# Performance work log

Measured on AMD Instinct MI355X. Metric: run time of the kernel, lower is better.

## Reference

```python
import jax, jax.numpy as jnp
import numpy as np

TOP_K = 2
NUM_MOE_LAYERS = 12


def _gemma_mlp(x, gate_w, up_w, down_w):
    # GemmaMLP: down( gelu_tanh(gate(x)) * up(x) )
    g = jnp.einsum('bsh,hi->bsi', x, gate_w)
    u = jnp.einsum('bsh,hi->bsi', x, up_w)
    return jnp.einsum('bsi,ih->bsh', jax.nn.gelu(g, approximate=True) * u, down_w)


def setup_inputs() -> dict:
    key = jax.random.key(0)
    ks = jax.random.split(key, 8)
    B, S, H, I, E = 32, 256, 1024, 4096, 8  # batch, seq, hidden, intermediate, skill experts
    std = 0.02
    return {
        'x': jax.random.normal(ks[0], (B, S, H), jnp.float32),
        'router_logits': jax.random.normal(ks[1], (B, E), jnp.float32),
        'skill_gate': jax.random.normal(ks[2], (E, H, I), jnp.float32) * std,
        'skill_up': jax.random.normal(ks[3], (E, H, I), jnp.float32) * std,
        'skill_down': jax.random.normal(ks[4], (E, I, H), jnp.float32) * std,
        'shared_gate': jax.random.normal(ks[5], (H, I), jnp.float32) * std,
        'shared_up': jax.random.normal(ks[6], (H, I), jnp.float32) * std,
        'shared_down': jax.random.normal(ks[7], (I, H), jnp.float32) * std,
    }


def reference(x, router_logits, skill_gate, skill_up, skill_down,
              shared_gate, shared_up, shared_down):
    B = x.shape[0]
    E = skill_gate.shape[0]
    # top-k softmax routing (per sequence), renormalized over selected experts
    rw = jax.nn.softmax(router_logits.astype(jnp.float32), axis=-1)
    w, sel = jax.lax.top_k(rw, TOP_K)                      # [B, k]
    w = w / w.sum(axis=-1, keepdims=True)
    w = w.astype(x.dtype)
    # ScaleGradient: identity fwd, grad scaled by 1/num_moe_layers
    scale = 1.0 / NUM_MOE_LAYERS
    w = scale * w + (1.0 - scale) * jax.lax.stop_gradient(w)
    # dense combine weights [B, E]; zero weight == not routed (same math as gather/scatter)
    dense_w = jnp.zeros((B, E), x.dtype).at[jnp.arange(B)[:, None], sel].add(w)

    def step(acc, params):
        g, u, d, we = params                               # we: [B]
        return acc + we[:, None, None] * _gemma_mlp(x, g, u, d), None

    out, _ = jax.lax.scan(step, jnp.zeros_like(x),
                          (skill_gate, skill_up, skill_down, dense_w.T))
    out = out + _gemma_mlp(x, shared_gate, shared_up, shared_down)
    return out
```

## Files before the change

kernel.cpp:

```cpp
#include <hip/hip_runtime.h>

typedef __bf16 bf16x8 __attribute__((ext_vector_type(8)));
typedef float  f32x4  __attribute__((ext_vector_type(4)));

__device__ __forceinline__ unsigned short f2bf(float f) {
    unsigned u = __float_as_uint(f);
    u += 0x7fffu + ((u >> 16) & 1u);
    return (unsigned short)(u >> 16);
}

__device__ __forceinline__ void gld_lds16(const void* g, void* l) {
    __builtin_amdgcn_global_load_lds(
        (const __attribute__((address_space(1))) void*)g,
        (__attribute__((address_space(3))) void*)l,
        16, 0, 0);
}

#define WAITVM(N) asm volatile("s_waitcnt vmcnt(" #N ")" ::: "memory")

#define NB  32
#define SQ  256
#define HD  1024
#define ID  4096
#define NEXP 8
#define PAIRS (NB * 3)

#define OFF_EID    ((size_t)0)
#define OFF_WGT    ((size_t)512)
#define OFF_XBF    ((size_t)1024)
#define OFF_GATET  (OFF_XBF   + (size_t)16777216)
#define OFF_UPT    (OFF_GATET + (size_t)75497472)
#define OFF_DOWNT  (OFF_UPT   + (size_t)75497472)
#define OFF_ACT    (OFF_DOWNT + (size_t)75497472)

__global__ void routing_kernel(const float* __restrict__ logits,
                               int* __restrict__ eid, float* __restrict__ wgt) {
    int b = threadIdx.x;
    if (b < NB) {
        float l[NEXP];
        for (int j = 0; j < NEXP; ++j) l[j] = logits[b * NEXP + j];
        int a0 = 0;
        for (int j = 1; j < NEXP; ++j) if (l[j] > l[a0]) a0 = j;
        int a1 = -1;
        for (int j = 0; j < NEXP; ++j) {
            if (j == a0) continue;
            if (a1 < 0 || l[j] > l[a1]) a1 = j;
        }
        float w0 = 1.0f / (1.0f + expf(l[a1] - l[a0]));
        eid[b * 3 + 0] = a0;  wgt[b * 3 + 0] = w0;
        eid[b * 3 + 1] = a1;  wgt[b * 3 + 1] = 1.0f - w0;
        eid[b * 3 + 2] = NEXP; wgt[b * 3 + 2] = 1.0f;
    }
}

__global__ void xcvt_kernel(const float* __restrict__ x,
                            unsigned short* __restrict__ xb, int n4) {
    int i = blockIdx.x * 256 + threadIdx.x;
    if (i < n4) {
        float4 v = ((const float4*)x)[i];
        union { unsigned short s[4]; uint2 u; } p;
        p.s[0] = f2bf(v.x); p.s[1] = f2bf(v.y);
        p.s[2] = f2bf(v.z); p.s[3] = f2bf(v.w);
        ((uint2*)xb)[i] = p.u;
    }
}

__global__ void transpose_cvt(const float* __restrict__ skill,
                              const float* __restrict__ shared_m,
                              unsigned short* __restrict__ out, int R, int C) {
    const int e = blockIdx.z;
    const float* src = (e < NEXP) ? (skill + (size_t)e * R * C) : shared_m;
    unsigned short* dst = out + (size_t)e * R * C;
    const int c0 = blockIdx.x * 64;
    const int r0 = blockIdx.y * 64;
    __shared__ unsigned short t[64][66];
    const int tid = threadIdx.x;
    const int lr = tid >> 4;
    const int lc = (tid & 15) * 4;
    for (int it = 0; it < 4; ++it) {
        int r = lr + it * 16;
        float4 v = *(const float4*)(src + (size_t)(r0 + r) * C + c0 + lc);
        t[r][lc + 0] = f2bf(v.x);
        t[r][lc + 1] = f2bf(v.y);
        t[r][lc + 2] = f2bf(v.z);
        t[r][lc + 3] = f2bf(v.w);
    }
    __syncthreads();
    const int oc = tid >> 2;
    const int k0 = (tid & 3) * 16;
    unsigned int pk[8];
    for (int j = 0; j < 8; ++j) {
        unsigned int lo = t[k0 + 2 * j + 0][oc];
        unsigned int hi = t[k0 + 2 * j + 1][oc];
        pk[j] = lo | (hi << 16);
    }
    unsigned short* dp = dst + (size_t)(c0 + oc) * R + r0 + k0;
    ((uint4*)dp)[0] = make_uint4(pk[0], pk[1], pk[2], pk[3]);
    ((uint4*)dp)[1] = make_uint4(pk[4], pk[5], pk[6], pk[7]);
}

__global__ __launch_bounds__(512, 2) void stage1_gateup(
    const unsigned short* __restrict__ xbf,
    const unsigned short* __restrict__ gateT,
    const unsigned short* __restrict__ upT,
    const int* __restrict__ eid, const float* __restrict__ wgt,
    unsigned short* __restrict__ act)
{
    extern __shared__ unsigned short lds[];

    const int lid = blockIdx.x;
    const int swz = (lid & 7) * 768 + (lid >> 3);
    const int nt  = swz & 31;
    const int mt  = (swz >> 5) & 1;
    const int p   = swz >> 6;
    const int b   = p / 3;
    const int e   = eid[p];
    const float wS = wgt[p];

    const int tid  = threadIdx.x;
    const int wv   = tid >> 6;
    const int lane = tid & 63;
    const int wr   = wv >> 2;
    const int wc   = wv & 3;

    const int lhi  = lane >> 3;
    const int llo  = lane & 7;
    const int csw8 = (llo ^ lhi) * 8;
    const int w2   = wv * 2;

    const size_t lofs = (size_t)(wv * 16 + lhi) * HD + csw8;
    const unsigned short* pA = xbf   + (size_t)(b * SQ + mt * 128) * HD + lofs;
    const unsigned short* pG = gateT + ((size_t)e * ID + nt * 128) * HD + lofs;
    const unsigned short* pU = upT   + ((size_t)e * ID + nt * 128) * HD + lofs;

    const int lrow = lane & 15;
    const int kq   = (lane >> 4) * 8;
    const int xt   = (lrow & 7) << 3;
    const int c0s  = kq ^ xt;
    const int c1s  = (32 + kq) ^ xt;
    const int rA0  = (wr * 64 + lrow) * 64;
    const int rG0  = (wc * 32 + lrow) * 64;

    f32x4 accg[4][2], accu[4][2];
#pragma unroll
    for (int i = 0; i < 4; ++i)
#pragma unroll
        for (int j = 0; j < 2; ++j) { accg[i][j] = (f32x4)0.f; accu[i][j] = (f32x4)0.f; }

    const int NT = HD / 64;

#pragma unroll
    for (int t0 = 0; t0 < 2; ++t0) {
        unsigned short* Lb = lds + t0 * 24576;
#pragma unroll
        for (int q = 0; q < 2; ++q) {
            const size_t o = (size_t)t0 * 64 + (size_t)q * (8 * HD);
            gld_lds16(pA + o, Lb +         (w2 + q) * 512);
            gld_lds16(pG + o, Lb +  8192 + (w2 + q) * 512);
            gld_lds16(pU + o, Lb + 16384 + (w2 + q) * 512);
        }
    }

    int cur = 0, tgt = 2;
#pragma unroll 1
    for (int t = 0; t < NT; ++t) {
        __builtin_amdgcn_sched_barrier(0);
        unsigned short* Lc = lds + cur * 24576;
        unsigned short* Lt = lds + tgt * 24576;
        const bool pf = (t + 2 < NT);
        const size_t kp = (size_t)(t + 2) * 64;
        if (pf) {
            gld_lds16(pA + kp, Lt +         w2 * 512);
            gld_lds16(pG + kp, Lt +  8192 + w2 * 512);
            gld_lds16(pU + kp, Lt + 16384 + w2 * 512);
            WAITVM(9);
        } else if (t + 1 < NT) {
            WAITVM(6);
        } else {
            WAITVM(0);
        }
        __builtin_amdgcn_s_barrier();
        __builtin_amdgcn_sched_barrier(0);

        {
            bf16x8 af[4], gf[2], uf[2];
#pragma unroll
            for (int mf = 0; mf < 4; ++mf)
                af[mf] = *(const bf16x8*)(Lc + rA0 + mf * 1024 + c0s);
#pragma unroll
            for (int nf = 0; nf < 2; ++nf) {
                gf[nf] = *(const bf16x8*)(Lc +  8192 + rG0 + nf * 1024 + c0s);
                uf[nf] = *(const bf16x8*)(Lc + 16384 + rG0 + nf * 1024 + c0s);
            }
            __builtin_amdgcn_s_setprio(1);
#pragma unroll
            for (int mf = 0; mf < 4; ++mf)
#pragma unroll
                for (int nf = 0; nf < 2; ++nf) {
                    accg[mf][nf] = __builtin_amdgcn_mfma_f32_16x16x32_bf16(af[mf], gf[nf], accg[mf][nf], 0, 0, 0);
                    accu[mf][nf] = __builtin_amdgcn_mfma_f32_16x16x32_bf16(af[mf], uf[nf], accu[mf][nf], 0, 0, 0);
                }
            __builtin_amdgcn_s_setprio(0);
        }
        __builtin_amdgcn_s_barrier();

        {
            bf16x8 af[4], gf[2], uf[2];
#pragma unroll
            for (int mf = 0; mf < 4; ++mf)
                af[mf] = *(const bf16x8*)(Lc + rA0 + mf * 1024 + c1s);
#pragma unroll
            for (int nf = 0; nf < 2; ++nf) {
                gf[nf] = *(const bf16x8*)(Lc +  8192 + rG0 + nf * 1024 + c1s);
                uf[nf] = *(const bf16x8*)(Lc + 16384 + rG0 + nf * 1024 + c1s);
            }
            if (pf) {
                gld_lds16(pA + kp + 8 * HD, Lt +         (w2 + 1) * 512);
                gld_lds16(pG + kp + 8 * HD, Lt +  8192 + (w2 + 1) * 512);
                gld_lds16(pU + kp + 8 * HD, Lt + 16384 + (w2 + 1) * 512);
            }
            __builtin_amdgcn_s_setprio(1);
#pragma unroll
            for (int mf = 0; mf < 4; ++mf)
#pragma unroll
                for (int nf = 0; nf < 2; ++nf) {
                    accg[mf][nf] = __builtin_amdgcn_mfma_f32_16x16x32_bf16(af[mf], gf[nf], accg[mf][nf], 0, 0, 0);
                    accu[mf][nf] = __builtin_amdgcn_mfma_f32_16x16x32_bf16(af[mf], uf[nf], accu[mf][nf], 0, 0, 0);
                }
            __builtin_amdgcn_s_setprio(0);
        }
        __builtin_amdgcn_s_barrier();

        cur = (cur == 2) ? 0 : cur + 1;
        tgt = (tgt == 2) ? 0 : tgt + 1;
    }

    unsigned short* actp = act + (size_t)p * (SQ * ID);
    const int rb = mt * 128 + wr * 64 + ((lane >> 4) << 2);
    const int cb = nt * 128 + wc * 32 + (lane & 15);
#pragma unroll
    for (int mf = 0; mf < 4; ++mf)
#pragma unroll
        for (int nf = 0; nf < 2; ++nf)
#pragma unroll
            for (int r = 0; r < 4; ++r) {
                float g = accg[mf][nf][r];
                float u = accu[mf][nf][r];
                float tt = 0.7978845608028654f * (g + 0.044715f * g * g * g);
                float h = 0.5f * g * (1.0f + tanhf(tt)) * u * wS;
                actp[(size_t)(rb + mf * 16 + r) * ID + cb + nf * 16] = f2bf(h);
            }
}

__global__ __launch_bounds__(512, 2) void stage2_down(
    const unsigned short* __restrict__ act,
    const unsigned short* __restrict__ downT,
    const int* __restrict__ eid,
    float* __restrict__ out)
{
    extern __shared__ unsigned short lds[];

    const int lid = blockIdx.x;
    const int swz = (lid & 7) * 32 + (lid >> 3);
    const int nt  = swz & 3;
    const int mt  = (swz >> 2) & 1;
    const int b   = swz >> 3;
    const int b3  = b * 3;
    const int e0 = eid[b3], e1 = eid[b3 + 1], e2 = eid[b3 + 2];

    const int tid  = threadIdx.x;
    const int wv   = tid >> 6;
    const int lane = tid & 63;
    const int wr   = wv >> 2;
    const int wc   = wv & 3;

    const int lhi  = lane >> 3;
    const int llo  = lane & 7;
    const int csw8 = (llo ^ lhi) * 8;
    const int w2   = wv * 2, w4 = wv * 4;

    const size_t laneA = (size_t)(wv * 16 + lhi) * ID + csw8;
    const size_t laneB = (size_t)(wv * 32 + lhi) * ID + csw8;

    const int lrow = lane & 15;
    const int kq   = (lane >> 4) * 8;
    const int xt   = (lrow & 7) << 3;
    const int c0s  = kq ^ xt;
    const int c1s  = (32 + kq) ^ xt;
    const int rA0  = (wr * 64 + lrow) * 64;
    const int rB0  = (wc * 64 + lrow) * 64;

    f32x4 acc[4][4];
#pragma unroll
    for (int i = 0; i < 4; ++i)
#pragma unroll
        for (int j = 0; j < 4; ++j) acc[i][j] = (f32x4)0.f;

    const int NT = 3 * ID / 64;

    auto srcAB = [&](int tt, const unsigned short*& A, const unsigned short*& B) {
        const int slot = tt >> 6;
        const int i0   = (tt & 63) << 6;
        const int esl  = (slot == 0) ? e0 : ((slot == 1) ? e1 : e2);
        A = act   + ((size_t)(b3 + slot) * SQ + mt * 128) * ID + i0 + laneA;
        B = downT + ((size_t)esl * HD + nt * 256) * ID + i0 + laneB;
    };

#pragma unroll
    for (int t0 = 0; t0 < 2; ++t0) {
        const unsigned short *A, *B;
        srcAB(t0, A, B);
        unsigned short* Lb = lds + t0 * 24576;
#pragma unroll
        for (int q = 0; q < 2; ++q)
            gld_lds16(A + (size_t)q * (8 * ID), Lb + (w2 + q) * 512);
#pragma unroll
        for (int q = 0; q < 4; ++q)
            gld_lds16(B + (size_t)q * (8 * ID), Lb + 8192 + (w4 + q) * 512);
    }

    int cur = 0, tgt = 2;
#pragma unroll 1
    for (int t = 0; t < NT; ++t) {
        __builtin_amdgcn_sched_barrier(0);
        unsigned short* Lc = lds + cur * 24576;
        unsigned short* Lt = lds + tgt * 24576;
        const bool pf = (t + 2 < NT);
        const unsigned short *SA = nullptr, *SB = nullptr;
        if (pf) {
            srcAB(t + 2, SA, SB);
            gld_lds16(SA,                    Lt +        w2 * 512);
            gld_lds16(SA + (size_t)(8 * ID), Lt +        (w2 + 1) * 512);
            gld_lds16(SB,                    Lt + 8192 + w4 * 512);
            WAITVM(9);
        } else if (t + 1 < NT) {
            WAITVM(6);
        } else {
            WAITVM(0);
        }
        __builtin_amdgcn_s_barrier();
        __builtin_amdgcn_sched_barrier(0);

        {
            bf16x8 af[4], bfr[4];
#pragma unroll
            for (int mf = 0; mf < 4; ++mf)
                af[mf] = *(const bf16x8*)(Lc + rA0 + mf * 1024 + c0s);
#pragma unroll
            for (int nf = 0; nf < 4; ++nf)
                bfr[nf] = *(const bf16x8*)(Lc + 8192 + rB0 + nf * 1024 + c0s);
            __builtin_amdgcn_s_setprio(1);
#pragma unroll
            for (int mf = 0; mf < 4; ++mf)
#pragma unroll
                for (int nf = 0; nf < 4; ++nf)
                    acc[mf][nf] = __builtin_amdgcn_mfma_f32_16x16x32_bf16(af[mf], bfr[nf], acc[mf][nf], 0, 0, 0);
            __builtin_amdgcn_s_setprio(0);
        }
        __builtin_amdgcn_s_barrier();

        {
            bf16x8 af[4], bfr[4];
#pragma unroll
            for (int mf = 0; mf < 4; ++mf)
                af[mf] = *(const bf16x8*)(Lc + rA0 + mf * 1024 + c1s);
#pragma unroll
            for (int nf = 0; nf < 4; ++nf)
                bfr[nf] = *(const bf16x8*)(Lc + 8192 + rB0 + nf * 1024 + c1s);
            if (pf) {
                gld_lds16(SB + (size_t)(8  * ID), Lt + 8192 + (w4 + 1) * 512);
                gld_lds16(SB + (size_t)(16 * ID), Lt + 8192 + (w4 + 2) * 512);
                gld_lds16(SB + (size_t)(24 * ID), Lt + 8192 + (w4 + 3) * 512);
            }
            __builtin_amdgcn_s_setprio(1);
#pragma unroll
            for (int mf = 0; mf < 4; ++mf)
#pragma unroll
                for (int nf = 0; nf < 4; ++nf)
                    acc[mf][nf] = __builtin_amdgcn_mfma_f32_16x16x32_bf16(af[mf], bfr[nf], acc[mf][nf], 0, 0, 0);
            __builtin_amdgcn_s_setprio(0);
        }
        __builtin_amdgcn_s_barrier();

        cur = (cur == 2) ? 0 : cur + 1;
        tgt = (tgt == 2) ? 0 : tgt + 1;
    }

    const int rb  = mt * 128 + wr * 64 + ((lane >> 4) << 2);
    const int cbN = nt * 256 + wc * 64 + (lane & 15);
#pragma unroll
    for (int mf = 0; mf < 4; ++mf)
#pragma unroll
        for (int nf = 0; nf < 4; ++nf)
#pragma unroll
            for (int r = 0; r < 4; ++r)
                out[((size_t)b * SQ + rb + mf * 16 + r) * HD + cbN + nf * 16] = acc[mf][nf][r];
}

extern "C" void kernel_launch(void* const* d_in, const int* in_sizes, int n_in,
                              void* d_out, int out_size, void* d_ws, size_t ws_size,
                              hipStream_t stream) {
    const float* x        = (const float*)d_in[0];
    const float* logits   = (const float*)d_in[1];
    const float* sk_gate  = (const float*)d_in[2];
    const float* sk_up    = (const float*)d_in[3];
    const float* sk_down  = (const float*)d_in[4];
    const float* sh_gate  = (const float*)d_in[5];
    const float* sh_up    = (const float*)d_in[6];
    const float* sh_down  = (const float*)d_in[7];
    float* out = (float*)d_out;

    char* ws = (char*)d_ws;
    int*            eid   = (int*)(ws + OFF_EID);
    float*          wgt   = (float*)(ws + OFF_WGT);
    unsigned short* xbf   = (unsigned short*)(ws + OFF_XBF);
    unsigned short* gateT = (unsigned short*)(ws + OFF_GATET);
    unsigned short* upT   = (unsigned short*)(ws + OFF_UPT);
    unsigned short* downT = (unsigned short*)(ws + OFF_DOWNT);
    unsigned short* act   = (unsigned short*)(ws + OFF_ACT);

    static int attr_set = 0;
    if (!attr_set) {
        hipFuncSetAttribute(reinterpret_cast<const void*>(stage1_gateup),
                            hipFuncAttributeMaxDynamicSharedMemorySize, 147456);
        hipFuncSetAttribute(reinterpret_cast<const void*>(stage2_down),
                            hipFuncAttributeMaxDynamicSharedMemorySize, 147456);
        attr_set = 1;
    }

    routing_kernel<<<1, 64, 0, stream>>>(logits, eid, wgt);

    const int n4 = (NB * SQ * HD) / 4;
    xcvt_kernel<<<(n4 + 255) / 256, 256, 0, stream>>>(x, xbf, n4);

    transpose_cvt<<<dim3(ID / 64, HD / 64, 9), 256, 0, stream>>>(sk_gate, sh_gate, gateT, HD, ID);
    transpose_cvt<<<dim3(ID / 64, HD / 64, 9), 256, 0, stream>>>(sk_up,   sh_up,   upT,   HD, ID);
    transpose_cvt<<<dim3(HD / 64, ID / 64, 9), 256, 0, stream>>>(sk_down, sh_down, downT, ID, HD);

    stage1_gateup<<<dim3(PAIRS * 64), 512, 147456, stream>>>(xbf, gateT, upT, eid, wgt, act);
    stage2_down<<<dim3(256), 512, 147456, stream>>>(act, downT, eid, out);
}
```

Baseline: 1.207 ms.

## Group stage1 blocks by expert and use exp-based GELU epilogue

The routing kernel now builds a counting-sort order of (batch, slot) pairs by expert id. Stage1 maps block indices through that order, so blocks resident on the same XCD group work on the same expert and can reuse its gate/up weights in L2. The GELU-tanh epilogue is rewritten as g*sigmoid(2t) using fast exp and divide, which replaces the tanhf call but gives slightly lower precision. A single thread does the sort serially, which adds a small fixed cost to the routing step.

```diff
diff --git a/kernel.cpp b/kernel.cpp
--- a/kernel.cpp
+++ b/kernel.cpp
@@ -32,6 +32,8 @@
 #define OFF_UPT    (OFF_GATET + (size_t)75497472)
 #define OFF_DOWNT  (OFF_UPT   + (size_t)75497472)
 #define OFF_ACT    (OFF_DOWNT + (size_t)75497472)
+
+__device__ int d_sord[PAIRS];
 
 __global__ void routing_kernel(const float* __restrict__ logits,
                                int* __restrict__ eid, float* __restrict__ wgt) {
@@ -50,6 +52,14 @@
         eid[b * 3 + 0] = a0;  wgt[b * 3 + 0] = w0;
         eid[b * 3 + 1] = a1;  wgt[b * 3 + 1] = 1.0f - w0;
         eid[b * 3 + 2] = NEXP; wgt[b * 3 + 2] = 1.0f;
+    }
+    __syncthreads();
+    if (threadIdx.x == 0) {
+        int cnt[NEXP + 2];
+        for (int i = 0; i < NEXP + 2; ++i) cnt[i] = 0;
+        for (int i = 0; i < PAIRS; ++i) cnt[eid[i] + 1]++;
+        for (int e = 0; e < NEXP + 1; ++e) cnt[e + 1] += cnt[e];
+        for (int i = 0; i < PAIRS; ++i) d_sord[cnt[eid[i]]++] = i;
     }
 }
 
@@ -108,13 +118,18 @@
 {
     extern __shared__ unsigned short lds[];
 
-    const int lid = blockIdx.x;
-    const int swz = (lid & 7) * 768 + (lid >> 3);
-    const int nt  = swz & 31;
-    const int mt  = (swz >> 5) & 1;
-    const int p   = swz >> 6;
-    const int b   = p / 3;
-    const int e   = eid[p];
+    const int bid = blockIdx.x;
+    const int g  = bid & 7;
+    const int r  = bid >> 3;
+    const int sg = r >> 8;
+    const int rr = r & 255;
+    const int nt = rr >> 3;
+    const int q  = rr & 7;
+    const int j  = g * 12 + sg * 4 + (q >> 1);
+    const int mt = q & 1;
+    const int p  = d_sord[j];
+    const int b  = p / 3;
+    const int e  = eid[p];
     const float wS = wgt[p];
 
     const int tid  = threadIdx.x;
@@ -145,7 +160,7 @@
 #pragma unroll
     for (int i = 0; i < 4; ++i)
 #pragma unroll
-        for (int j = 0; j < 2; ++j) { accg[i][j] = (f32x4)0.f; accu[i][j] = (f32x4)0.f; }
+        for (int jj = 0; jj < 2; ++jj) { accg[i][jj] = (f32x4)0.f; accu[i][jj] = (f32x4)0.f; }
 
     const int NT = HD / 64;
 
@@ -153,11 +168,11 @@
     for (int t0 = 0; t0 < 2; ++t0) {
         unsigned short* Lb = lds + t0 * 24576;
 #pragma unroll
-        for (int q = 0; q < 2; ++q) {
-            const size_t o = (size_t)t0 * 64 + (size_t)q * (8 * HD);
-            gld_lds16(pA + o, Lb +         (w2 + q) * 512);
-            gld_lds16(pG + o, Lb +  8192 + (w2 + q) * 512);
-            gld_lds16(pU + o, Lb + 16384 + (w2 + q) * 512);
+        for (int qq = 0; qq < 2; ++qq) {
+            const size_t o = (size_t)t0 * 64 + (size_t)qq * (8 * HD);
+            gld_lds16(pA + o, Lb +         (w2 + qq) * 512);
+            gld_lds16(pG + o, Lb +  8192 + (w2 + qq) * 512);
+            gld_lds16(pU + o, Lb + 16384 + (w2 + qq) * 512);
         }
     }
 
@@ -243,12 +258,12 @@
 #pragma unroll
         for (int nf = 0; nf < 2; ++nf)
 #pragma unroll
-            for (int r = 0; r < 4; ++r) {
-                float g = accg[mf][nf][r];
-                float u = accu[mf][nf][r];
-                float tt = 0.7978845608028654f * (g + 0.044715f * g * g * g);
-                float h = 0.5f * g * (1.0f + tanhf(tt)) * u * wS;
-                actp[(size_t)(rb + mf * 16 + r) * ID + cb + nf * 16] = f2bf(h);
+            for (int r2 = 0; r2 < 4; ++r2) {
+                float gv = accg[mf][nf][r2];
+                float uv = accu[mf][nf][r2];
+                float t2 = -1.5957691216057308f * gv * (1.0f + 0.044715f * gv * gv);
+                float h  = __fdividef(gv, 1.0f + __expf(t2)) * uv * wS;
+                actp[(size_t)(rb + mf * 16 + r2) * ID + cb + nf * 16] = f2bf(h);
             }
 }
 
```

Result: faster. 1.122 ms (-7.1%).
